# Kernel tuning notes

Measured on AMD Instinct MI355X. Metric: run time of the kernel, lower is better.

The kernel has to match this reference:

```python
import jax, jax.numpy as jnp
import numpy as np

N_NODES = 100000
TYPE_COUNTS = [40000, 40000, 20000]
RAW_DIMS = [512, 256, 128]
D = 64          # node_feature_dim
H = 8           # num_attention_heads
M = 2           # num_metapaths
E = 500000      # edges per metapath
SEM = 128       # semantic_attention_dim
NUM_CLS = 8
T = 40000       # num target nodes
SLOPE = 0.01    # leaky relu slope


def setup_inputs() -> dict:
    key = jax.random.key(0)
    ks = jax.random.split(key, 16)
    inp = {}
    inp['target_nodes'] = jax.random.randint(ks[0], (T,), 0, N_NODES)
    inp['metapath_0'] = jax.random.randint(ks[1], (E, 2), 0, N_NODES)
    inp['metapath_1'] = jax.random.randint(ks[2], (E, 2), 0, N_NODES)
    # contiguous blocks per node type (type t occupies a contiguous index range)
    inp['node_type_mapping'] = jnp.concatenate(
        [jnp.full((c,), t, dtype=jnp.int32) for t, c in enumerate(TYPE_COUNTS)])
    for t, (c, r) in enumerate(zip(TYPE_COUNTS, RAW_DIMS)):
        inp[f'node_feat_{t}'] = jax.random.normal(ks[3 + t], (c, r), dtype=jnp.float32)
        xav = float(np.sqrt(2.0) * np.sqrt(2.0 / (D + r)))
        inp[f'W{t}'] = jax.random.normal(ks[6 + t], (D, r), dtype=jnp.float32) * xav
        inp[f'b{t}'] = jnp.zeros((D,), dtype=jnp.float32)
    inp['node_attention'] = jax.random.normal(ks[9], (M, H, 2 * D), dtype=jnp.float32) * 0.05
    inp['Wsem'] = jax.random.normal(ks[10], (SEM, H * D), dtype=jnp.float32) * 0.05
    inp['bsem'] = jnp.zeros((SEM,), dtype=jnp.float32)
    inp['a_sem'] = jax.random.normal(ks[11], (SEM,), dtype=jnp.float32) * 0.05
    inp['Wcls'] = jax.random.normal(ks[12], (NUM_CLS, H * D), dtype=jnp.float32) * 0.05
    inp['bcls'] = jnp.zeros((NUM_CLS,), dtype=jnp.float32)
    return inp


def _metapath_agg(node_features, mp, attn_vec, target_nodes, n_nodes):
    # mp: [E, 2] (col 0 = neighbor/src, col -1 = current/dst); attn_vec: [H, 2D]
    src = mp[:, 0]
    dst = mp[:, -1]
    h_src = node_features[src]                        # [E, D] gather
    h_dst = node_features[dst]                        # [E, D] gather
    e = jnp.concatenate([h_dst, h_src], axis=-1)      # [E, 2D]
    score = e @ attn_vec.T                            # [E, H]
    score = jnp.where(score > 0, score, SLOPE * score)  # LeakyReLU
    # edge softmax over incoming edges of each destination node (per head)
    m = jax.ops.segment_max(score, dst, num_segments=n_nodes)
    ex = jnp.exp(score - m[dst])
    den = jax.ops.segment_sum(ex, dst, num_segments=n_nodes)
    attn = ex / den[dst]                              # [E, H]
    weighted = h_src[:, None, :] * attn[:, :, None]   # [E, H, D]
    agg = jax.ops.segment_sum(weighted, dst, num_segments=n_nodes)  # [N, H, D]
    return agg[target_nodes]                          # [T, H, D]


def reference(target_nodes, metapath_0, metapath_1, node_type_mapping,
              node_feat_0, node_feat_1, node_feat_2,
              W0, b0, W1, b1, W2, b2,
              node_attention, Wsem, bsem, a_sem, Wcls, bcls):
    n_nodes = node_type_mapping.shape[0]
    # node types are contiguous index blocks, so per-type projection + concat
    # reproduces the original scatter-by-type exactly (dropout rate is 0)
    node_features = jnp.concatenate([
        node_feat_0 @ W0.T + b0,
        node_feat_1 @ W1.T + b1,
        node_feat_2 @ W2.T + b2,
    ], axis=0)                                        # [N, D]
    h_list = [
        _metapath_agg(node_features, metapath_0, node_attention[0], target_nodes, n_nodes),
        _metapath_agg(node_features, metapath_1, node_attention[1], target_nodes, n_nodes),
    ]
    h = jnp.stack(h_list).reshape(M, -1, H * D)       # [M, T, H*D]
    s = jnp.tanh(jnp.einsum('mtd,sd->mts', h, Wsem) + bsem)  # [M, T, SEM]
    scores = jnp.mean(s @ a_sem, axis=1)              # [M] semantic attention
    beta = jax.nn.softmax(scores)                     # [M]
    embeddings = jnp.einsum('m,mtd->td', beta, h)     # [T, H*D]
    cls_logits = embeddings @ Wcls.T + bcls           # [T, NUM_CLS]
    return cls_logits, embeddings
```

## Files before the change

kernel.cpp:

```cpp
#include <hip/hip_runtime.h>
#include <hip/hip_bf16.h>

#define N_NODES 100000
#define EDGES   500000
#define T_TGT   40000
#define NH      8
#define NSEM    128
#define NCLS    8
#define SLOPE   0.01f
#define NCHUNK  25

typedef __attribute__((ext_vector_type(8))) __bf16 bf16x8;
typedef __attribute__((ext_vector_type(4))) float f32x4;

__global__ __launch_bounds__(256) void proj_gemm(const float* __restrict__ A,
        const float* __restrict__ W, const float* __restrict__ bias,
        float* __restrict__ out, int M, int K) {
    __shared__ float As[32][68];
    __shared__ float Ws[32][68];
    int tid = threadIdx.x;
    int r0 = blockIdx.x * 64;
    int ty = tid >> 4;
    int tx = tid & 15;
    float acc[4][4] = {};
    for (int kk = 0; kk < K; kk += 32) {
        #pragma unroll
        for (int i = 0; i < 2; i++) {
            int lin = tid + i * 256;
            int row = lin >> 3;
            int c4 = (lin & 7) * 4;
            float4 v = make_float4(0.f, 0.f, 0.f, 0.f);
            if (r0 + row < M)
                v = *(const float4*)(A + (size_t)(r0 + row) * K + kk + c4);
            As[c4 + 0][row] = v.x; As[c4 + 1][row] = v.y;
            As[c4 + 2][row] = v.z; As[c4 + 3][row] = v.w;
            float4 w = *(const float4*)(W + (size_t)row * K + kk + c4);
            Ws[c4 + 0][row] = w.x; Ws[c4 + 1][row] = w.y;
            Ws[c4 + 2][row] = w.z; Ws[c4 + 3][row] = w.w;
        }
        __syncthreads();
        #pragma unroll
        for (int k = 0; k < 32; k++) {
            float4 a4 = *(const float4*)&As[k][ty * 4];
            float4 b4 = *(const float4*)&Ws[k][tx * 4];
            float a[4] = {a4.x, a4.y, a4.z, a4.w};
            float b[4] = {b4.x, b4.y, b4.z, b4.w};
            #pragma unroll
            for (int i = 0; i < 4; i++)
                #pragma unroll
                for (int j = 0; j < 4; j++)
                    acc[i][j] = fmaf(a[i], b[j], acc[i][j]);
        }
        __syncthreads();
    }
    float4 b4 = *(const float4*)(bias + tx * 4);
    #pragma unroll
    for (int i = 0; i < 4; i++) {
        int r = r0 + ty * 4 + i;
        if (r < M) {
            float4 o = make_float4(acc[i][0] + b4.x, acc[i][1] + b4.y,
                                   acc[i][2] + b4.z, acc[i][3] + b4.w);
            *(float4*)(out + (size_t)r * 64 + tx * 4) = o;
        }
    }
}

__global__ __launch_bounds__(256) void attn_proj(const float* __restrict__ nf,
        const float* __restrict__ na, float* __restrict__ proj) {
    __shared__ float ft[64][65];
    __shared__ float at[32][65];
    int tid = threadIdx.x;
    int n0 = blockIdx.x * 64;
    #pragma unroll
    for (int i = 0; i < 8; i++) {
        int lin = tid + i * 256;
        int j = lin >> 6, d = lin & 63;
        int m = j >> 4, side = (j >> 3) & 1, h = j & 7;
        at[j][d] = na[m * 1024 + h * 128 + side * 64 + d];
    }
    #pragma unroll
    for (int i = 0; i < 4; i++) {
        int lin = tid + i * 256;
        int row = lin >> 4;
        int c4 = (lin & 15) * 4;
        int gn = n0 + row;
        float4 v = make_float4(0.f, 0.f, 0.f, 0.f);
        if (gn < N_NODES) v = *(const float4*)(nf + (size_t)gn * 64 + c4);
        ft[row][c4 + 0] = v.x; ft[row][c4 + 1] = v.y;
        ft[row][c4 + 2] = v.z; ft[row][c4 + 3] = v.w;
    }
    __syncthreads();
    int node = tid >> 2;
    int jg = tid & 3;
    float acc[8] = {};
    for (int d = 0; d < 64; d++) {
        float f = ft[node][d];
        #pragma unroll
        for (int jj = 0; jj < 8; jj++)
            acc[jj] = fmaf(f, at[jg * 8 + jj][d], acc[jj]);
    }
    int gn = n0 + node;
    if (gn < N_NODES) {
        float4 o0 = make_float4(acc[0], acc[1], acc[2], acc[3]);
        float4 o1 = make_float4(acc[4], acc[5], acc[6], acc[7]);
        *(float4*)(proj + (size_t)gn * 32 + jg * 8) = o0;
        *(float4*)(proj + (size_t)gn * 32 + jg * 8 + 4) = o1;
    }
}

__global__ void hist_targets(const int* __restrict__ tgt, int* __restrict__ tcnt) {
    int i = blockIdx.x * 256 + threadIdx.x;
    if (i < T_TGT) atomicAdd(&tcnt[tgt[i]], 1);
}

__global__ void hist_edges(const int* __restrict__ mp, const int* __restrict__ tcnt,
                           int* __restrict__ ecnt) {
    int e = blockIdx.x * 256 + threadIdx.x;
    if (e < EDGES) {
        int dst = mp[2 * e + 1];
        if (tcnt[dst] > 0) atomicAdd(&ecnt[dst], 1);
    }
}

__global__ __launch_bounds__(1024) void scan_partial(const int* __restrict__ counts,
        int* __restrict__ partials) {
    int a = blockIdx.y, bx = blockIdx.x;
    const int* in = counts + (size_t)a * N_NODES;
    int base = bx * 4096 + threadIdx.x * 4;
    int s = 0;
    #pragma unroll
    for (int i = 0; i < 4; i++) {
        int idx = base + i;
        if (idx < N_NODES) s += in[idx];
    }
    #pragma unroll
    for (int off = 32; off; off >>= 1) s += __shfl_xor(s, off);
    __shared__ int red[16];
    int lane = threadIdx.x & 63, w = threadIdx.x >> 6;
    if (lane == 0) red[w] = s;
    __syncthreads();
    if (threadIdx.x < 16) {
        int x = red[threadIdx.x];
        #pragma unroll
        for (int off = 8; off; off >>= 1) x += __shfl_xor(x, off);
        if (threadIdx.x == 0) partials[a * 32 + bx] = x;
    }
}

__global__ void scan_partials(const int* __restrict__ partials,
        int* __restrict__ choff, int* __restrict__ offs) {
    int w = threadIdx.x >> 6, lane = threadIdx.x & 63;
    if (w < 3 && lane < 32) {
        int v = (lane < NCHUNK) ? partials[w * 32 + lane] : 0;
        int x = v;
        #pragma unroll
        for (int off = 1; off < 32; off <<= 1) {
            int y = __shfl_up(x, off);
            if (lane >= off) x += y;
        }
        if (lane < NCHUNK) choff[w * 32 + lane] = x - v;
        if (lane == NCHUNK - 1) offs[(size_t)w * (N_NODES + 1) + N_NODES] = x;
    }
}

__global__ __launch_bounds__(1024) void scan_final(const int* __restrict__ counts,
        const int* __restrict__ choff, int* __restrict__ offs, int* __restrict__ curs) {
    int a = blockIdx.y, bx = blockIdx.x;
    const int* in = counts + (size_t)a * N_NODES;
    int* out = offs + (size_t)a * (N_NODES + 1);
    int* cur = curs + (size_t)a * N_NODES;
    int tid = threadIdx.x, lane = tid & 63, w = tid >> 6;
    int base = bx * 4096 + tid * 4;
    int v[4], sum4 = 0;
    #pragma unroll
    for (int i = 0; i < 4; i++) {
        int idx = base + i;
        v[i] = (idx < N_NODES) ? in[idx] : 0;
        sum4 += v[i];
    }
    int x = sum4;
    #pragma unroll
    for (int off = 1; off < 64; off <<= 1) {
        int y = __shfl_up(x, off);
        if (lane >= off) x += y;
    }
    __shared__ int wred[16], wexc[16];
    if (lane == 63) wred[w] = x;
    __syncthreads();
    if (tid < 16) {
        int s = wred[tid], xs = s;
        #pragma unroll
        for (int off = 1; off < 16; off <<= 1) {
            int y = __shfl_up(xs, off);
            if (tid >= off) xs += y;
        }
        wexc[tid] = xs - s;
    }
    __syncthreads();
    int off0 = choff[a * 32 + bx] + wexc[w] + (x - sum4);
    int run = 0;
    #pragma unroll
    for (int i = 0; i < 4; i++) {
        int idx = base + i;
        if (idx < N_NODES) { out[idx] = off0 + run; cur[idx] = off0 + run; }
        run += v[i];
    }
}

__global__ void scatter_targets(const int* __restrict__ tgt, int* __restrict__ tcur,
                                int* __restrict__ tlist) {
    int i = blockIdx.x * 256 + threadIdx.x;
    if (i < T_TGT) {
        int n = tgt[i];
        int p = atomicAdd(&tcur[n], 1);
        tlist[p] = i;
    }
}

__global__ __launch_bounds__(256) void scatter_score(const int* __restrict__ mp,
        const int* __restrict__ tcnt, int* __restrict__ ecur,
        int* __restrict__ elist, __bf16* __restrict__ exs,
        const float* __restrict__ proj, int m) {
    int e = blockIdx.x * 256 + threadIdx.x;
    if (e >= EDGES) return;
    int src = mp[2 * e], dst = mp[2 * e + 1];
    if (tcnt[dst] <= 0) return;
    int p = atomicAdd(&ecur[dst], 1);
    elist[p] = src;
    const float* adp = proj + (size_t)dst * 32 + m * 16;
    const float* asp = proj + (size_t)src * 32 + m * 16 + 8;
    float4 ad0 = *(const float4*)(adp), ad1 = *(const float4*)(adp + 4);
    float4 as0 = *(const float4*)(asp), as1 = *(const float4*)(asp + 4);
    float ads[8] = {ad0.x, ad0.y, ad0.z, ad0.w, ad1.x, ad1.y, ad1.z, ad1.w};
    float ass[8] = {as0.x, as0.y, as0.z, as0.w, as1.x, as1.y, as1.z, as1.w};
    bf16x8 exv;
    #pragma unroll
    for (int h = 0; h < 8; h++) {
        float sc = ads[h] + ass[h];
        sc = sc > 0.f ? sc : SLOPE * sc;
        exv[h] = (__bf16)__expf(sc);
    }
    *(bf16x8*)(exs + (size_t)p * 8) = exv;
}

__global__ void build_ulist(const int* __restrict__ tcnt, int* __restrict__ ulist,
                            int* __restrict__ ucount) {
    int n = blockIdx.x * 256 + threadIdx.x;
    if (n < N_NODES && tcnt[n] > 0) {
        int u = atomicAdd(ucount, 1);
        ulist[u] = n;
    }
}

__global__ void cvt_bf16(const float* __restrict__ in, __bf16* __restrict__ out, int n) {
    int i = blockIdx.x * 256 + threadIdx.x;
    if (i < n) out[i] = (__bf16)in[i];
}

__global__ __launch_bounds__(256) void agg_kernel(
        const int* __restrict__ ulist, const int* __restrict__ ctrl_i,
        const int* __restrict__ offs,
        const int* __restrict__ esrc,
        const __bf16* __restrict__ exs,
        const float* __restrict__ nf,
        const int* __restrict__ tlist,
        __bf16* hb0, __bf16* hb1) {
    int m = blockIdx.y;
    int wslot = blockIdx.x * 4 + (threadIdx.x >> 6);
    int lane = threadIdx.x & 63;
    int ucount = ctrl_i[0];
    if (wslot >= ucount) return;
    int node = __builtin_amdgcn_readfirstlane(ulist[wslot]);
    const int* eo = offs + (size_t)m * (N_NODES + 1);
    int e0 = eo[node], e1 = eo[node + 1];
    const int* srcs = esrc + (size_t)m * EDGES;
    const __bf16* exm = exs + (size_t)m * EDGES * 8;
    float acc[8] = {};
    float dacc[8] = {};
    for (int e = e0; e < e1; e++) {
        int s = srcs[e];
        bf16x8 pb = *(const bf16x8*)(exm + (size_t)e * 8);
        float v = nf[(size_t)s * 64 + lane];
        #pragma unroll
        for (int h = 0; h < 8; h++) {
            float pw = (float)pb[h];
            dacc[h] += pw;
            acc[h] = fmaf(pw, v, acc[h]);
        }
    }
    #pragma unroll
    for (int h = 0; h < 8; h++)
        acc[h] *= (dacc[h] > 0.f) ? 1.0f / dacc[h] : 0.f;
    const int* to = offs + (size_t)2 * (N_NODES + 1);
    int t0 = to[node], t1 = to[node + 1];
    __bf16* hb = (m == 0) ? hb0 : hb1;
    for (int ti = t0; ti < t1; ti++) {
        int t = tlist[ti];
        __bf16* dst = hb + (size_t)t * 512;
        #pragma unroll
        for (int h = 0; h < 8; h++) dst[h * 64 + lane] = (__bf16)acc[h];
    }
}

__global__ __launch_bounds__(256) void sem_mfma(
        const __bf16* __restrict__ hb,
        const __bf16* __restrict__ Wb,
        const float* __restrict__ bsem, const float* __restrict__ a_sem,
        float* __restrict__ scores) {
    int m = blockIdx.y;
    const __bf16* A = hb + (size_t)m * T_TGT * 512 + (size_t)blockIdx.x * 64 * 512;
    int wave = threadIdx.x >> 6, lane = threadIdx.x & 63;
    int n0 = wave * 32;
    int mrow = lane & 15;
    int koff0 = (lane >> 4) * 8;
    f32x4 acc[4][2] = {};
    for (int k0 = 0; k0 < 512; k0 += 32) {
        int koff = k0 + koff0;
        bf16x8 a[4], b[2];
        #pragma unroll
        for (int r = 0; r < 4; r++)
            a[r] = *(const bf16x8*)(A + (size_t)(r * 16 + mrow) * 512 + koff);
        #pragma unroll
        for (int c = 0; c < 2; c++)
            b[c] = *(const bf16x8*)(Wb + (size_t)(n0 + c * 16 + mrow) * 512 + koff);
        #pragma unroll
        for (int r = 0; r < 4; r++)
            #pragma unroll
            for (int c = 0; c < 2; c++)
                acc[r][c] = __builtin_amdgcn_mfma_f32_16x16x32_bf16(a[r], b[c], acc[r][c], 0, 0, 0);
    }
    float tot = 0.f;
    #pragma unroll
    for (int c = 0; c < 2; c++) {
        int col = n0 + c * 16 + (lane & 15);
        float bs = bsem[col], as = a_sem[col];
        #pragma unroll
        for (int r = 0; r < 4; r++)
            #pragma unroll
            for (int j = 0; j < 4; j++) {
                float x = acc[r][c][j] + bs;
                float th = 1.f - 2.f / (__expf(2.f * x) + 1.f);
                tot += th * as;
            }
    }
    __shared__ float red[256];
    red[threadIdx.x] = tot;
    __syncthreads();
    for (int s = 128; s; s >>= 1) {
        if (threadIdx.x < s) red[threadIdx.x] += red[threadIdx.x + s];
        __syncthreads();
    }
    if (threadIdx.x == 0) atomicAdd(&scores[m], red[0]);
}

__global__ void beta_kernel(const float* __restrict__ scores, float* __restrict__ beta) {
    if (threadIdx.x == 0) {
        float s0 = scores[0] / (float)T_TGT;
        float s1 = scores[1] / (float)T_TGT;
        float mx = fmaxf(s0, s1);
        float e0 = __expf(s0 - mx), e1 = __expf(s1 - mx);
        float inv = 1.f / (e0 + e1);
        beta[0] = e0 * inv;
        beta[1] = e1 * inv;
    }
}

__global__ __launch_bounds__(256) void emb_cls(
        const __bf16* __restrict__ hb0, const __bf16* __restrict__ hb1,
        const float* __restrict__ beta, const float* __restrict__ Wcls,
        const float* __restrict__ bcls, float* out_cls, float* out_emb) {
    __shared__ float Wl[8 * 512];
    int tid = threadIdx.x;
    #pragma unroll
    for (int i = 0; i < 16; i++) Wl[tid + i * 256] = Wcls[tid + i * 256];
    __syncthreads();
    int t = blockIdx.x * 4 + (tid >> 6);
    int lane = tid & 63;
    float b0 = beta[0], b1 = beta[1];
    bf16x8 v0 = *(const bf16x8*)(hb0 + (size_t)t * 512 + lane * 8);
    bf16x8 v1 = *(const bf16x8*)(hb1 + (size_t)t * 512 + lane * 8);
    float e[8];
    #pragma unroll
    for (int j = 0; j < 8; j++) e[j] = b0 * (float)v0[j] + b1 * (float)v1[j];
    float* ep = out_emb + (size_t)t * 512 + lane * 8;
    *(float4*)(ep + 0) = make_float4(e[0], e[1], e[2], e[3]);
    *(float4*)(ep + 4) = make_float4(e[4], e[5], e[6], e[7]);
    float pc[8];
    #pragma unroll
    for (int c = 0; c < 8; c++) {
        float4 w0 = *(const float4*)(Wl + c * 512 + lane * 8);
        float4 w1 = *(const float4*)(Wl + c * 512 + lane * 8 + 4);
        pc[c] = e[0] * w0.x + e[1] * w0.y + e[2] * w0.z + e[3] * w0.w
              + e[4] * w1.x + e[5] * w1.y + e[6] * w1.z + e[7] * w1.w;
    }
    #pragma unroll
    for (int off = 32; off; off >>= 1)
        #pragma unroll
        for (int c = 0; c < 8; c++) pc[c] += __shfl_xor(pc[c], off);
    if (lane == 0) {
        #pragma unroll
        for (int c = 0; c < 8; c++) out_cls[(size_t)t * 8 + c] = pc[c] + bcls[c];
    }
}

extern "C" void kernel_launch(void* const* d_in, const int* in_sizes, int n_in,
                              void* d_out, int out_size, void* d_ws, size_t ws_size,
                              hipStream_t stream) {
    const int* target = (const int*)d_in[0];
    const int* mp0 = (const int*)d_in[1];
    const int* mp1 = (const int*)d_in[2];
    const float* feat0 = (const float*)d_in[4];
    const float* W0 = (const float*)d_in[5];
    const float* b0 = (const float*)d_in[6];
    const float* feat1 = (const float*)d_in[7];
    const float* W1 = (const float*)d_in[8];
    const float* b1 = (const float*)d_in[9];
    const float* feat2 = (const float*)d_in[10];
    const float* W2 = (const float*)d_in[11];
    const float* b2 = (const float*)d_in[12];
    const float* natt = (const float*)d_in[13];
    const float* Wsem = (const float*)d_in[14];
    const float* bsem = (const float*)d_in[15];
    const float* asem = (const float*)d_in[16];
    const float* Wcls = (const float*)d_in[17];
    const float* bcls = (const float*)d_in[18];

    char* ws = (char*)d_ws;
    size_t off = 0;
    auto alloc = [&](size_t bytes) -> void* {
        void* p = ws + off;
        off += (bytes + 31) & ~(size_t)31;
        return p;
    };
    float* nf    = (float*)alloc((size_t)N_NODES * 64 * 4);
    float* proj  = (float*)alloc((size_t)N_NODES * 32 * 4);
    int* counts3 = (int*)alloc((size_t)3 * N_NODES * 4);
    int* offs3   = (int*)alloc((size_t)3 * (N_NODES + 1) * 4);
    int* curs3   = (int*)alloc((size_t)3 * N_NODES * 4);
    int* tlist   = (int*)alloc((size_t)T_TGT * 4);
    int* ulist   = (int*)alloc((size_t)N_NODES * 4);
    int* esrc    = (int*)alloc((size_t)2 * EDGES * 4);
    __bf16* exs  = (__bf16*)alloc((size_t)2 * EDGES * 8 * 2);
    int* partials = (int*)alloc((size_t)3 * 32 * 4);
    int* choff    = (int*)alloc((size_t)3 * 32 * 4);
    int* ctrl    = (int*)alloc(64);
    __bf16* Wsem_b = (__bf16*)alloc((size_t)NSEM * 512 * 2);
    __bf16* hb   = (__bf16*)alloc((size_t)2 * T_TGT * 512 * 2);
    if (off > ws_size) return;

    float* out_cls = (float*)d_out;
    float* out_emb = out_cls + (size_t)T_TGT * NCLS;
    __bf16* hb0 = hb;
    __bf16* hb1 = hb + (size_t)T_TGT * 512;
    float* ctrl_f = (float*)ctrl;
    float* scores = ctrl_f + 1;
    float* beta = ctrl_f + 3;

    hipMemsetAsync(counts3, 0, (size_t)3 * N_NODES * 4, stream);
    hipMemsetAsync(ctrl, 0, 64, stream);

    proj_gemm<<<dim3(625), 256, 0, stream>>>(feat0, W0, b0, nf, 40000, 512);
    proj_gemm<<<dim3(625), 256, 0, stream>>>(feat1, W1, b1, nf + (size_t)40000 * 64, 40000, 256);
    proj_gemm<<<dim3(313), 256, 0, stream>>>(feat2, W2, b2, nf + (size_t)80000 * 64, 20000, 128);
    attn_proj<<<dim3(1563), 256, 0, stream>>>(nf, natt, proj);
    cvt_bf16<<<dim3(256), 256, 0, stream>>>(Wsem, Wsem_b, NSEM * 512);

    hist_targets<<<dim3(157), 256, 0, stream>>>(target, counts3 + 2 * N_NODES);
    hist_edges<<<dim3(1954), 256, 0, stream>>>(mp0, counts3 + 2 * N_NODES, counts3);
    hist_edges<<<dim3(1954), 256, 0, stream>>>(mp1, counts3 + 2 * N_NODES, counts3 + N_NODES);
    scan_partial<<<dim3(NCHUNK, 3), 1024, 0, stream>>>(counts3, partials);
    scan_partials<<<dim3(1), 192, 0, stream>>>(partials, choff, offs3);
    scan_final<<<dim3(NCHUNK, 3), 1024, 0, stream>>>(counts3, choff, offs3, curs3);
    scatter_targets<<<dim3(157), 256, 0, stream>>>(target, curs3 + 2 * N_NODES, tlist);
    scatter_score<<<dim3(1954), 256, 0, stream>>>(mp0, counts3 + 2 * N_NODES, curs3,
                                                  esrc, exs, proj, 0);
    scatter_score<<<dim3(1954), 256, 0, stream>>>(mp1, counts3 + 2 * N_NODES, curs3 + N_NODES,
                                                  esrc + EDGES, exs + (size_t)EDGES * 8, proj, 1);
    build_ulist<<<dim3(391), 256, 0, stream>>>(counts3 + 2 * N_NODES, ulist, ctrl);

    agg_kernel<<<dim3(10000, 2), 256, 0, stream>>>(ulist, ctrl, offs3, esrc, exs,
                                                   nf, tlist, hb0, hb1);
    sem_mfma<<<dim3(625, 2), 256, 0, stream>>>(hb, Wsem_b, bsem, asem, scores);
    beta_kernel<<<dim3(1), 64, 0, stream>>>(scores, beta);
    emb_cls<<<dim3(10000), 256, 0, stream>>>(hb0, hb1, beta, Wcls, bcls, out_cls, out_emb);
}
```

Before: 524.9 us.

## Stage semantic GEMM tiles in LDS with async double-buffered global loads

The semantic-attention MFMA kernel now loads A and W tiles into shared memory with global_load_lds (direct global-to-LDS) and double buffering over 64-wide K chunks, instead of each wave reading its operands straight from global memory. The goal is to share the A tile across the four waves, which previously each re-read all 64 rows, and to overlap the next tile's loads with the current MFMAs. In exchange it adds LDS traffic, unpadded LDS rows that may cause bank conflicts, and a barrier per K step. Synchronisation depends on __syncthreads waiting for the async LDS loads to finish.

After: 515.5 us. No clear change (-1.8%).

```diff
diff --git a/kernel.cpp b/kernel.cpp
--- a/kernel.cpp
+++ b/kernel.cpp
@@ -9,6 +9,9 @@
 #define NCLS    8
 #define SLOPE   0.01f
 #define NCHUNK  25
+
+#define AS1 __attribute__((address_space(1)))
+#define AS3 __attribute__((address_space(3)))
 
 typedef __attribute__((ext_vector_type(8))) __bf16 bf16x8;
 typedef __attribute__((ext_vector_type(4))) float f32x4;
@@ -307,28 +310,67 @@
         const __bf16* __restrict__ Wb,
         const float* __restrict__ bsem, const float* __restrict__ a_sem,
         float* __restrict__ scores) {
+    __shared__ __bf16 As[2][64 * 64];
+    __shared__ __bf16 Bs[2][128 * 64];
     int m = blockIdx.y;
-    const __bf16* A = hb + (size_t)m * T_TGT * 512 + (size_t)blockIdx.x * 64 * 512;
-    int wave = threadIdx.x >> 6, lane = threadIdx.x & 63;
-    int n0 = wave * 32;
+    int tid = threadIdx.x;
+    int wave = tid >> 6, lane = tid & 63;
+    const __bf16* A0 = hb + (size_t)m * T_TGT * 512 + (size_t)blockIdx.x * 64 * 512;
+
+    int srow = lane >> 3;
+    int scol = (lane & 7) * 8;
+
+    auto stage = [&](int buf, int k0) {
+        #pragma unroll
+        for (int j = 0; j < 2; j++) {
+            int row = j * 32 + wave * 8 + srow;
+            const __bf16* gp = A0 + (size_t)row * 512 + k0 + scol;
+            __bf16* lp = &As[buf][(j * 32 + wave * 8) * 64];
+            __builtin_amdgcn_global_load_lds((const AS1 void*)gp,
+                                             (AS3 void*)lp, 16, 0, 0);
+        }
+        #pragma unroll
+        for (int j = 0; j < 4; j++) {
+            int row = j * 32 + wave * 8 + srow;
+            const __bf16* gp = Wb + (size_t)row * 512 + k0 + scol;
+            __bf16* lp = &Bs[buf][(j * 32 + wave * 8) * 64];
+            __builtin_amdgcn_global_load_lds((const AS1 void*)gp,
+                                             (AS3 void*)lp, 16, 0, 0);
+        }
+    };
+
     int mrow = lane & 15;
-    int koff0 = (lane >> 4) * 8;
+    int kq = lane >> 4;
     f32x4 acc[4][2] = {};
-    for (int k0 = 0; k0 < 512; k0 += 32) {
-        int koff = k0 + koff0;
-        bf16x8 a[4], b[2];
-        #pragma unroll
-        for (int r = 0; r < 4; r++)
-            a[r] = *(const bf16x8*)(A + (size_t)(r * 16 + mrow) * 512 + koff);
-        #pragma unroll
-        for (int c = 0; c < 2; c++)
-            b[c] = *(const bf16x8*)(Wb + (size_t)(n0 + c * 16 + mrow) * 512 + koff);
-        #pragma unroll
-        for (int r = 0; r < 4; r++)
+
+    stage(0, 0);
+    __syncthreads();
+    for (int t = 0; t < 8; t++) {
+        int cur = t & 1;
+        if (t < 7) stage(cur ^ 1, (t + 1) * 64);
+        __builtin_amdgcn_sched_barrier(0);
+        const __bf16* Ab = &As[cur][0];
+        const __bf16* Bb = &Bs[cur][0];
+        #pragma unroll
+        for (int kk = 0; kk < 2; kk++) {
+            int ko = kk * 32 + kq * 8;
+            bf16x8 a[4], b[2];
+            #pragma unroll
+            for (int r = 0; r < 4; r++)
+                a[r] = *(const bf16x8*)(Ab + (r * 16 + mrow) * 64 + ko);
             #pragma unroll
             for (int c = 0; c < 2; c++)
-                acc[r][c] = __builtin_amdgcn_mfma_f32_16x16x32_bf16(a[r], b[c], acc[r][c], 0, 0, 0);
-    }
+                b[c] = *(const bf16x8*)(Bb + (wave * 32 + c * 16 + mrow) * 64 + ko);
+            #pragma unroll
+            for (int r = 0; r < 4; r++)
+                #pragma unroll
+                for (int c = 0; c < 2; c++)
+                    acc[r][c] = __builtin_amdgcn_mfma_f32_16x16x32_bf16(a[r], b[c], acc[r][c], 0, 0, 0);
+        }
+        __syncthreads();
+    }
+
+    int n0 = wave * 32;
     float tot = 0.f;
     #pragma unroll
     for (int c = 0; c < 2; c++) {
```
